# Optimization experiments

Measured on AMD Instinct MI355X. Metric: run time of the kernel, lower is better.

The kernel has to match this reference:

```python
import jax, jax.numpy as jnp
import numpy as np

B, H, S, Dqk, Dv = 4, 16, 2048, 64, 64
HID = 1024  # hidden_dim; v_tot_dim = H*Dv = 1024


def setup_inputs() -> dict:
    key = jax.random.key(0)
    kq, kk, kv, kw = jax.random.split(key, 4)
    return {
        "q": jax.random.normal(kq, (B, H, S, Dqk), dtype=jnp.float32),
        "k": jax.random.normal(kk, (B, H, S, Dqk), dtype=jnp.float32),
        "v": jax.random.normal(kv, (B, H, S, Dv), dtype=jnp.float32),
        "attention_mask": jnp.zeros((B, H, S, S), dtype=jnp.float32),
        "W_proj": jax.random.normal(kw, (HID, H * Dv), dtype=jnp.float32) * 0.02,
    }


def reference(q, k, v, attention_mask, W_proj):
    # scores: [B, H, S, S] -- explicitly materialized, as in the original
    scores = jnp.einsum("bhqd,bhkd->bhqk", q, k) + attention_mask
    attn = jax.nn.softmax(scores, axis=-1)
    # attn @ v -> [B, H, S, Dv]
    out = jnp.einsum("bhqk,bhkd->bhqd", attn, v)
    # rearrange '... h l d -> ... l (h d)'
    out = jnp.transpose(out, (0, 2, 1, 3)).reshape(B, S, H * Dv)
    # Linear(bias=False): y = x @ W^T
    out = out @ W_proj.T
    return (out, attn)
```

## Files before the change

kernel.cpp:

```cpp
#include <hip/hip_runtime.h>
#include <hip/hip_bf16.h>

#define BB 4
#define HH 16
#define SS 2048
#define DD 64
#define HIDD 1024
#define NBH (BB * HH)
#define EQK (NBH * SS * DD)
#define LOG2E 1.44269504088896f
#define M2C 57.7078016f

typedef __attribute__((ext_vector_type(4))) float f32x4;
typedef __attribute__((ext_vector_type(8))) short bf16x8;

__device__ __forceinline__ short f2bf(float x) {
    union { float f; unsigned u; } v; v.f = x;
    return (short)((v.u + 0x7FFFu + ((v.u >> 16) & 1u)) >> 16);
}
__device__ __forceinline__ float bf2f(short b) {
    union { float f; unsigned u; } v;
    v.u = ((unsigned)(unsigned short)b) << 16;
    return v.f;
}
__device__ __forceinline__ f32x4 mfma16(bf16x8 a, bf16x8 b, f32x4 c) {
    return __builtin_amdgcn_mfma_f32_16x16x32_bf16(a, b, c, 0, 0, 0);
}
__device__ __forceinline__ float fexp2(float x) { return __builtin_amdgcn_exp2f(x); }

__global__ __launch_bounds__(256) void prep_split(const float* __restrict__ k,
                                                  short* __restrict__ hi,
                                                  short* __restrict__ lo) {
    int t = blockIdx.x * 256 + threadIdx.x;
    int lane = t & 63, h = (t >> 6) & 1, kt = (t >> 7) & 127, bh = t >> 14;
    int r16 = lane & 15, gl = lane >> 4;
    int s = kt * 16 + r16, d0 = h * 32 + gl * 8;
    const float* src = k + ((size_t)bh * SS + s) * DD + d0;
    bf16x8 hh, ll;
#pragma unroll
    for (int j = 0; j < 8; ++j) {
        float x = src[j];
        short hb = f2bf(x);
        hh[j] = hb;
        ll[j] = f2bf(x - bf2f(hb));
    }
    *(bf16x8*)(hi + (size_t)t * 8) = hh;
    *(bf16x8*)(lo + (size_t)t * 8) = ll;
}

__global__ __launch_bounds__(256) void prep_cast(const float* __restrict__ src,
                                                 short* __restrict__ dst, int n8) {
    int i = blockIdx.x * 256 + threadIdx.x;
    if (i >= n8) return;
    const float* p = src + (size_t)i * 8;
    bf16x8 h;
#pragma unroll
    for (int j = 0; j < 8; ++j) h[j] = f2bf(p[j]);
    *(bf16x8*)(dst + (size_t)i * 8) = h;
}

__global__ __launch_bounds__(256) void vt_kernel(const float* __restrict__ v,
                                                 short* __restrict__ vT) {
    int t = blockIdx.x * 256 + threadIdx.x;
    int lane = t & 63, cc = (t >> 6) & 63, dt = (t >> 12) & 3, bh = t >> 14;
    int r16 = lane & 15, gl = lane >> 4;
    const float* src = v + ((size_t)bh * SS + cc * 32 + gl * 8) * DD + dt * 16 + r16;
    bf16x8 o;
#pragma unroll
    for (int j = 0; j < 8; ++j) o[j] = f2bf(src[(size_t)j * DD]);
    *(bf16x8*)(vT + (size_t)t * 8) = o;
}

template <int PLAN>
__global__ __launch_bounds__(256) void attn_sweep(
    const float* __restrict__ q,
    const short* __restrict__ khi, const short* __restrict__ klo,
    const float* __restrict__ mask, const short* __restrict__ vT,
    short* __restrict__ Pout, float* __restrict__ attn_raw,
    float* __restrict__ lrow, short* __restrict__ pvb16) {
    __shared__ short pbuf[4][2][16][40];
    const int w = threadIdx.x >> 6;
    const int lane = threadIdx.x & 63;
    const int r16 = lane & 15, g = lane >> 4;
    const int bid = blockIdx.x;
    const int swz = (bid & 7) * 256 + (bid >> 3);
    const int bh = swz >> 5;
    const int q0 = (swz & 31) * 64 + w * 16;

    const float* qrow = q + ((size_t)bh * SS + q0 + r16) * DD + g * 8;
    bf16x8 qh0, ql0, qh1, ql1;
#pragma unroll
    for (int j = 0; j < 8; ++j) {
        float x0 = qrow[j];
        short h0 = f2bf(x0); qh0[j] = h0; ql0[j] = f2bf(x0 - bf2f(h0));
        float x1 = qrow[32 + j];
        short h1 = f2bf(x1); qh1[j] = h1; ql1[j] = f2bf(x1 - bf2f(h1));
    }

    const short* kb = khi + (size_t)bh * 131072;
    const short* lb = klo + (size_t)bh * 131072;
    const float* mb = mask + ((size_t)bh * SS + q0) * SS;
    const short* vtb = vT + (size_t)bh * 131072;
    short* Pb = Pout + ((size_t)bh * SS + q0) * SS + (size_t)r16 * SS;
    float* ab = attn_raw + ((size_t)bh * SS + q0) * SS;

    float l[4] = {0.f, 0.f, 0.f, 0.f};
    f32x4 opv[4];
#pragma unroll
    for (int dt = 0; dt < 4; ++dt) opv[dt] = f32x4{0.f, 0.f, 0.f, 0.f};

    auto loadk = [&](bf16x8 (&KH)[4], bf16x8 (&KL)[4], float (&MK)[8], int ccv) {
        const short* kc = kb + (size_t)ccv * 2048 + lane * 8;
        const short* lc = lb + (size_t)ccv * 2048 + lane * 8;
#pragma unroll
        for (int u = 0; u < 4; ++u) {
            KH[u] = *(const bf16x8*)(kc + u * 512);
            KL[u] = *(const bf16x8*)(lc + u * 512);
        }
        const float* mrow = mb + ccv * 32;
#pragma unroll
        for (int i = 0; i < 4; ++i) {
            MK[2 * i]     = mrow[(size_t)(g * 4 + i) * SS + r16];
            MK[2 * i + 1] = mrow[(size_t)(g * 4 + i) * SS + 16 + r16];
        }
    };

    auto body = [&](bf16x8 (&KH)[4], bf16x8 (&KL)[4], float (&MK)[8], int ccv, int pb) {
        f32x4 a0 = {0.f, 0.f, 0.f, 0.f}, a1 = {0.f, 0.f, 0.f, 0.f};
        a0 = mfma16(qh0, KH[0], a0); a1 = mfma16(qh0, KH[2], a1);
        a0 = mfma16(ql0, KH[0], a0); a1 = mfma16(ql0, KH[2], a1);
        a0 = mfma16(qh0, KL[0], a0); a1 = mfma16(qh0, KL[2], a1);
        a0 = mfma16(qh1, KH[1], a0); a1 = mfma16(qh1, KH[3], a1);
        a0 = mfma16(ql1, KH[1], a0); a1 = mfma16(ql1, KH[3], a1);
        a0 = mfma16(qh1, KL[1], a0); a1 = mfma16(qh1, KL[3], a1);
#pragma unroll
        for (int i = 0; i < 4; ++i) {
            float c0 = __builtin_fmaf(MK[2 * i], LOG2E, -M2C);
            float c1 = __builtin_fmaf(MK[2 * i + 1], LOG2E, -M2C);
            float p0 = fexp2(__builtin_fmaf(a0[i], LOG2E, c0));
            float p1 = fexp2(__builtin_fmaf(a1[i], LOG2E, c1));
            l[i] += p0 + p1;
            if constexpr (PLAN == 1) {
                ab[(size_t)(g * 4 + i) * SS + ccv * 32 + r16] = p0;
                ab[(size_t)(g * 4 + i) * SS + ccv * 32 + 16 + r16] = p1;
            }
            pbuf[w][pb][g * 4 + i][r16] = f2bf(p0);
            pbuf[w][pb][g * 4 + i][16 + r16] = f2bf(p1);
        }
        bf16x8 pf = *(const bf16x8*)&pbuf[w][pb][r16][g * 8];
        if constexpr (PLAN == 0) {
            *(bf16x8*)(Pb + ccv * 32 + g * 8) = pf;
        }
#pragma unroll
        for (int dt = 0; dt < 4; ++dt) {
            bf16x8 vf = *(const bf16x8*)(vtb + ((size_t)dt * 64 + ccv) * 512 + lane * 8);
            opv[dt] = mfma16(pf, vf, opv[dt]);
        }
    };

    bf16x8 KhA[4], KlA[4], KhB[4], KlB[4];
    float mkA[8], mkB[8];
    loadk(KhA, KlA, mkA, 0);
    for (int cc = 0; cc < 64; cc += 2) {
        loadk(KhB, KlB, mkB, cc + 1);
        body(KhA, KlA, mkA, cc, 0);
        if (cc + 2 < 64) loadk(KhA, KlA, mkA, cc + 2);
        body(KhB, KlB, mkB, cc + 1, 1);
    }

    float linv[4];
#pragma unroll
    for (int i = 0; i < 4; ++i) {
#pragma unroll
        for (int off = 1; off < 16; off <<= 1) l[i] += __shfl_xor(l[i], off, 64);
        linv[i] = 1.0f / l[i];
    }
    if (r16 == 0) {
#pragma unroll
        for (int i = 0; i < 4; ++i) lrow[(size_t)bh * SS + q0 + g * 4 + i] = linv[i];
    }

    short* pvo = pvb16 + ((size_t)bh * SS + q0) * DD;
#pragma unroll
    for (int dt = 0; dt < 4; ++dt)
#pragma unroll
        for (int i = 0; i < 4; ++i)
            pvo[(size_t)(g * 4 + i) * DD + dt * 16 + r16] = f2bf(opv[dt][i] * linv[i]);
}

__global__ __launch_bounds__(256) void rescale_a(const short* __restrict__ P,
                                                 const float* __restrict__ lrow,
                                                 float* __restrict__ attn) {
    size_t t = (size_t)blockIdx.x * 256 + threadIdx.x;
    size_t row = t >> 8;
    int c0 = (int)(t & 255) << 3;
    float s = lrow[row];
    bf16x8 p = *(const bf16x8*)(P + row * SS + c0);
    float4 o0, o1;
    o0.x = bf2f(p[0]) * s; o0.y = bf2f(p[1]) * s; o0.z = bf2f(p[2]) * s; o0.w = bf2f(p[3]) * s;
    o1.x = bf2f(p[4]) * s; o1.y = bf2f(p[5]) * s; o1.z = bf2f(p[6]) * s; o1.w = bf2f(p[7]) * s;
    float* d = attn + row * SS + c0;
    *(float4*)d = o0;
    *(float4*)(d + 4) = o1;
}

__global__ __launch_bounds__(256) void rescale_b(float* __restrict__ attn,
                                                 const float* __restrict__ lrow) {
    size_t t = (size_t)blockIdx.x * 256 + threadIdx.x;
    size_t row = t >> 8;
    int c0 = (int)(t & 255) << 3;
    float s = lrow[row];
    float* d = attn + row * SS + c0;
    float4 a = *(float4*)d, b = *(float4*)(d + 4);
    a.x *= s; a.y *= s; a.z *= s; a.w *= s;
    b.x *= s; b.y *= s; b.z *= s; b.w *= s;
    *(float4*)d = a;
    *(float4*)(d + 4) = b;
}

__global__ __launch_bounds__(256) void proj_kernel(const short* __restrict__ xb,
                                                   const short* __restrict__ wb,
                                                   float* __restrict__ out) {
    const int w = threadIdx.x >> 6;
    const int lane = threadIdx.x & 63;
    const int r16 = lane & 15, g = lane >> 4;
    const int ww = blockIdx.x * 4 + w;
    const int nb = ww >> 4;
    const int ob = ww & 15;
    const int n0 = nb * 16;
    const int n = n0 + r16;
    const int b = n >> 11, s = n & (SS - 1);

    f32x4 acc[4];
#pragma unroll
    for (int ot = 0; ot < 4; ++ot) acc[ot] = f32x4{0.f, 0.f, 0.f, 0.f};

    for (int kk = 0; kk < HIDD / 32; ++kk) {
        const int c = kk * 32 + g * 8;
        const int h = c >> 6, d = c & 63;
        bf16x8 af = *(const bf16x8*)(xb + ((size_t)(b * HH + h) * SS + s) * DD + d);
#pragma unroll
        for (int ot = 0; ot < 4; ++ot) {
            const int o = (ob * 64) + ot * 16 + r16;
            bf16x8 bf = *(const bf16x8*)(wb + (size_t)o * HIDD + c);
            acc[ot] = mfma16(af, bf, acc[ot]);
        }
    }
#pragma unroll
    for (int ot = 0; ot < 4; ++ot)
#pragma unroll
        for (int i = 0; i < 4; ++i)
            out[(size_t)(n0 + g * 4 + i) * HIDD + (ob * 64) + ot * 16 + r16] = acc[ot][i];
}

extern "C" void kernel_launch(void* const* d_in, const int* in_sizes, int n_in,
                              void* d_out, int out_size, void* d_ws, size_t ws_size,
                              hipStream_t stream) {
    const float* q   = (const float*)d_in[0];
    const float* k   = (const float*)d_in[1];
    const float* v   = (const float*)d_in[2];
    const float* msk = (const float*)d_in[3];
    const float* Wp  = (const float*)d_in[4];

    float* out = (float*)d_out;
    float* attn_out = out + (size_t)BB * SS * HIDD;

    char* ws = (char*)d_ws;
    size_t off = 0;
    short* vT  = (short*)(ws + off); off += (size_t)EQK * 2;
    short* khi = (short*)(ws + off); off += (size_t)EQK * 2;
    short* klo = (short*)(ws + off); off += (size_t)EQK * 2;
    short* wbf = (short*)(ws + off); off += (size_t)HIDD * HIDD * 2;
    short* pvb = (short*)(ws + off); off += (size_t)EQK * 2;
    float* lrw = (float*)(ws + off); off += (size_t)NBH * SS * 4;
    short* Pbf = (short*)(ws + off);
    size_t needA = off + (size_t)NBH * SS * SS * 2;
    const bool planA = (ws_size >= needA);

    prep_split<<<EQK / 8 / 256, 256, 0, stream>>>(k, khi, klo);
    prep_cast<<<HIDD * HIDD / 8 / 256, 256, 0, stream>>>(Wp, wbf, HIDD * HIDD / 8);
    vt_kernel<<<EQK / 8 / 256, 256, 0, stream>>>(v, vT);

    const int rsblocks = (int)(((size_t)NBH * SS * SS / 8) / 256);
    if (planA) {
        attn_sweep<0><<<NBH * (SS / 64), 256, 0, stream>>>(
            q, khi, klo, msk, vT, Pbf, (float*)ws, lrw, pvb);
        rescale_a<<<rsblocks, 256, 0, stream>>>(Pbf, lrw, attn_out);
    } else {
        attn_sweep<1><<<NBH * (SS / 64), 256, 0, stream>>>(
            q, khi, klo, msk, vT, (short*)ws, attn_out, lrw, pvb);
        rescale_b<<<rsblocks, 256, 0, stream>>>(attn_out, lrw);
    }
    proj_kernel<<<(BB * SS / 16) * (HIDD / 64) / 4, 256, 0, stream>>>(pvb, wbf, out);
}
```

Measured before the change: 1.041 ms.

## Transpose QK MFMA to row-per-lane layout, replace LDS P staging with shuffles

Swaps the MFMA operand order so each lane holds four consecutive key columns of one query row. The mask can then be loaded with float4 and fed in as the accumulator init, and the attn and P stores become contiguous vector writes. The LDS round trip that re-laid out P for the PV MFMA is replaced by cross-lane shuffles, and the QK product is split into two independent accumulator chains. Row-sum reduction simplifies, and launch bounds now request two blocks per CU, which risks register spills.

```diff
diff --git a/kernel.cpp b/kernel.cpp
--- a/kernel.cpp
+++ b/kernel.cpp
@@ -23,6 +23,9 @@
     v.u = ((unsigned)(unsigned short)b) << 16;
     return v.f;
 }
+__device__ __forceinline__ int pk2(float a, float b) {
+    return ((int)(unsigned short)f2bf(b) << 16) | (int)(unsigned short)f2bf(a);
+}
 __device__ __forceinline__ f32x4 mfma16(bf16x8 a, bf16x8 b, f32x4 c) {
     return __builtin_amdgcn_mfma_f32_16x16x32_bf16(a, b, c, 0, 0, 0);
 }
@@ -72,13 +75,12 @@
 }
 
 template <int PLAN>
-__global__ __launch_bounds__(256) void attn_sweep(
+__global__ __launch_bounds__(256, 2) void attn_sweep(
     const float* __restrict__ q,
     const short* __restrict__ khi, const short* __restrict__ klo,
     const float* __restrict__ mask, const short* __restrict__ vT,
     short* __restrict__ Pout, float* __restrict__ attn_raw,
     float* __restrict__ lrow, short* __restrict__ pvb16) {
-    __shared__ short pbuf[4][2][16][40];
     const int w = threadIdx.x >> 6;
     const int lane = threadIdx.x & 63;
     const int r16 = lane & 15, g = lane >> 4;
@@ -99,93 +101,106 @@
 
     const short* kb = khi + (size_t)bh * 131072;
     const short* lb = klo + (size_t)bh * 131072;
-    const float* mb = mask + ((size_t)bh * SS + q0) * SS;
+    const float* mrow = mask + ((size_t)bh * SS + q0 + r16) * SS;
     const short* vtb = vT + (size_t)bh * 131072;
-    short* Pb = Pout + ((size_t)bh * SS + q0) * SS + (size_t)r16 * SS;
-    float* ab = attn_raw + ((size_t)bh * SS + q0) * SS;
-
-    float l[4] = {0.f, 0.f, 0.f, 0.f};
-    f32x4 opv[4];
-#pragma unroll
-    for (int dt = 0; dt < 4; ++dt) opv[dt] = f32x4{0.f, 0.f, 0.f, 0.f};
-
-    auto loadk = [&](bf16x8 (&KH)[4], bf16x8 (&KL)[4], float (&MK)[8], int ccv) {
+    short* Pb = Pout + ((size_t)bh * SS + q0 + r16) * SS;
+    float* ab = attn_raw + ((size_t)bh * SS + q0 + r16) * SS;
+
+    float lsum = 0.f;
+    f32x4 opv0 = {0.f,0.f,0.f,0.f}, opv1 = {0.f,0.f,0.f,0.f};
+    f32x4 opv2 = {0.f,0.f,0.f,0.f}, opv3 = {0.f,0.f,0.f,0.f};
+
+    auto LK = [&](bf16x8 (&KH)[4], bf16x8 (&KL)[4], float4& mk0, float4& mk1, int ccv) {
         const short* kc = kb + (size_t)ccv * 2048 + lane * 8;
         const short* lc = lb + (size_t)ccv * 2048 + lane * 8;
-#pragma unroll
-        for (int u = 0; u < 4; ++u) {
-            KH[u] = *(const bf16x8*)(kc + u * 512);
-            KL[u] = *(const bf16x8*)(lc + u * 512);
+        KH[0] = *(const bf16x8*)(kc);        KH[1] = *(const bf16x8*)(kc + 512);
+        KH[2] = *(const bf16x8*)(kc + 1024); KH[3] = *(const bf16x8*)(kc + 1536);
+        KL[0] = *(const bf16x8*)(lc);        KL[1] = *(const bf16x8*)(lc + 512);
+        KL[2] = *(const bf16x8*)(lc + 1024); KL[3] = *(const bf16x8*)(lc + 1536);
+        const float* mp = mrow + ccv * 32 + 4 * g;
+        mk0 = *(const float4*)(mp);
+        mk1 = *(const float4*)(mp + 16);
+    };
+
+    auto BODY = [&](bf16x8 (&KH)[4], bf16x8 (&KL)[4], float4 mk0, float4 mk1, int ccv) {
+        const short* vc = vtb + (size_t)ccv * 512 + lane * 8;
+        bf16x8 vf0 = *(const bf16x8*)(vc);
+        bf16x8 vf1 = *(const bf16x8*)(vc + 32768);
+        bf16x8 vf2 = *(const bf16x8*)(vc + 65536);
+        bf16x8 vf3 = *(const bf16x8*)(vc + 98304);
+        f32x4 c00 = {mk0.x, mk0.y, mk0.z, mk0.w};
+        f32x4 c10 = {mk1.x, mk1.y, mk1.z, mk1.w};
+        f32x4 c01 = {0.f,0.f,0.f,0.f}, c11 = {0.f,0.f,0.f,0.f};
+        c00 = mfma16(KH[0], qh0, c00);  c01 = mfma16(KH[1], qh1, c01);
+        c10 = mfma16(KH[2], qh0, c10);  c11 = mfma16(KH[3], qh1, c11);
+        c00 = mfma16(KL[0], qh0, c00);  c01 = mfma16(KL[1], qh1, c01);
+        c10 = mfma16(KL[2], qh0, c10);  c11 = mfma16(KL[3], qh1, c11);
+        c00 = mfma16(KH[0], ql0, c00);  c01 = mfma16(KH[1], ql1, c01);
+        c10 = mfma16(KH[2], ql0, c10);  c11 = mfma16(KH[3], ql1, c11);
+        float p0[4], p1[4];
+#pragma unroll
+        for (int i = 0; i < 4; ++i) {
+            p0[i] = fexp2(__builtin_fmaf(c00[i] + c01[i], LOG2E, -M2C));
+            p1[i] = fexp2(__builtin_fmaf(c10[i] + c11[i], LOG2E, -M2C));
         }
-        const float* mrow = mb + ccv * 32;
-#pragma unroll
-        for (int i = 0; i < 4; ++i) {
-            MK[2 * i]     = mrow[(size_t)(g * 4 + i) * SS + r16];
-            MK[2 * i + 1] = mrow[(size_t)(g * 4 + i) * SS + 16 + r16];
+        lsum += (p0[0] + p0[1]) + (p0[2] + p0[3]) + (p1[0] + p1[1]) + (p1[2] + p1[3]);
+        if constexpr (PLAN == 1) {
+            float4 s0 = {p0[0], p0[1], p0[2], p0[3]};
+            float4 s1 = {p1[0], p1[1], p1[2], p1[3]};
+            *(float4*)(ab + ccv * 32 + 4 * g) = s0;
+            *(float4*)(ab + ccv * 32 + 16 + 4 * g) = s1;
         }
-    };
-
-    auto body = [&](bf16x8 (&KH)[4], bf16x8 (&KL)[4], float (&MK)[8], int ccv, int pb) {
-        f32x4 a0 = {0.f, 0.f, 0.f, 0.f}, a1 = {0.f, 0.f, 0.f, 0.f};
-        a0 = mfma16(qh0, KH[0], a0); a1 = mfma16(qh0, KH[2], a1);
-        a0 = mfma16(ql0, KH[0], a0); a1 = mfma16(ql0, KH[2], a1);
-        a0 = mfma16(qh0, KL[0], a0); a1 = mfma16(qh0, KL[2], a1);
-        a0 = mfma16(qh1, KH[1], a0); a1 = mfma16(qh1, KH[3], a1);
-        a0 = mfma16(ql1, KH[1], a0); a1 = mfma16(ql1, KH[3], a1);
-        a0 = mfma16(qh1, KL[1], a0); a1 = mfma16(qh1, KL[3], a1);
-#pragma unroll
-        for (int i = 0; i < 4; ++i) {
-            float c0 = __builtin_fmaf(MK[2 * i], LOG2E, -M2C);
-            float c1 = __builtin_fmaf(MK[2 * i + 1], LOG2E, -M2C);
-            float p0 = fexp2(__builtin_fmaf(a0[i], LOG2E, c0));
-            float p1 = fexp2(__builtin_fmaf(a1[i], LOG2E, c1));
-            l[i] += p0 + p1;
-            if constexpr (PLAN == 1) {
-                ab[(size_t)(g * 4 + i) * SS + ccv * 32 + r16] = p0;
-                ab[(size_t)(g * 4 + i) * SS + ccv * 32 + 16 + r16] = p1;
-            }
-            pbuf[w][pb][g * 4 + i][r16] = f2bf(p0);
-            pbuf[w][pb][g * 4 + i][16 + r16] = f2bf(p1);
-        }
-        bf16x8 pf = *(const bf16x8*)&pbuf[w][pb][r16][g * 8];
+        int e0 = pk2(p0[0], p0[1]), e1 = pk2(p0[2], p0[3]);
+        int e2 = pk2(p1[0], p1[1]), e3 = pk2(p1[2], p1[3]);
+        int f0 = __shfl_xor(e0, 16), f1 = __shfl_xor(e1, 16);
+        int f2 = __shfl_xor(e2, 16), f3 = __shfl_xor(e3, 16);
+        const bool ge = (g & 1) == 0;
+        int L0 = ge ? e0 : f0, L1 = ge ? e1 : f1, L2 = ge ? f0 : e0, L3 = ge ? f1 : e1;
+        int H0 = ge ? e2 : f2, H1 = ge ? e3 : f3, H2 = ge ? f2 : e2, H3 = ge ? f3 : e3;
+        const bool lo2 = g < 2;
+        int r0 = __shfl_xor(lo2 ? H0 : L0, 32);
+        int r1 = __shfl_xor(lo2 ? H1 : L1, 32);
+        int r2 = __shfl_xor(lo2 ? H2 : L2, 32);
+        int r3 = __shfl_xor(lo2 ? H3 : L3, 32);
+        union { int i4[4]; bf16x8 v; } ua;
+        ua.i4[0] = (g == 0) ? L0 : (g == 3) ? H0 : r0;
+        ua.i4[1] = (g == 0) ? L1 : (g == 3) ? H1 : r1;
+        ua.i4[2] = (g == 0) ? L2 : (g == 3) ? H2 : r2;
+        ua.i4[3] = (g == 0) ? L3 : (g == 3) ? H3 : r3;
+        bf16x8 pf = ua.v;
         if constexpr (PLAN == 0) {
             *(bf16x8*)(Pb + ccv * 32 + g * 8) = pf;
         }
-#pragma unroll
-        for (int dt = 0; dt < 4; ++dt) {
-            bf16x8 vf = *(const bf16x8*)(vtb + ((size_t)dt * 64 + ccv) * 512 + lane * 8);
-            opv[dt] = mfma16(pf, vf, opv[dt]);
-        }
+        opv0 = mfma16(pf, vf0, opv0);
+        opv1 = mfma16(pf, vf1, opv1);
+        opv2 = mfma16(pf, vf2, opv2);
+        opv3 = mfma16(pf, vf3, opv3);
     };
 
     bf16x8 KhA[4], KlA[4], KhB[4], KlB[4];
-    float mkA[8], mkB[8];
-    loadk(KhA, KlA, mkA, 0);
+    float4 mA0, mA1, mB0, mB1;
+    LK(KhA, KlA, mA0, mA1, 0);
     for (int cc = 0; cc < 64; cc += 2) {
-        loadk(KhB, KlB, mkB, cc + 1);
-        body(KhA, KlA, mkA, cc, 0);
-        if (cc + 2 < 64) loadk(KhA, KlA, mkA, cc + 2);
-        body(KhB, KlB, mkB, cc + 1, 1);
-    }
-
-    float linv[4];
+        LK(KhB, KlB, mB0, mB1, cc + 1);
+        BODY(KhA, KlA, mA0, mA1, cc);
+        if (cc + 2 < 64) LK(KhA, KlA, mA0, mA1, cc + 2);
+        BODY(KhB, KlB, mB0, mB1, cc + 1);
+    }
+
+    lsum += __shfl_xor(lsum, 16);
+    lsum += __shfl_xor(lsum, 32);
+    const float linv = 1.0f / lsum;
+    if (g == 0) lrow[(size_t)bh * SS + q0 + r16] = linv;
+
+    short* pvo = pvb16 + ((size_t)bh * SS + q0) * DD;
 #pragma unroll
     for (int i = 0; i < 4; ++i) {
-#pragma unroll
-        for (int off = 1; off < 16; off <<= 1) l[i] += __shfl_xor(l[i], off, 64);
-        linv[i] = 1.0f / l[i];
-    }
-    if (r16 == 0) {
-#pragma unroll
-        for (int i = 0; i < 4; ++i) lrow[(size_t)bh * SS + q0 + g * 4 + i] = linv[i];
-    }
-
-    short* pvo = pvb16 + ((size_t)bh * SS + q0) * DD;
-#pragma unroll
-    for (int dt = 0; dt < 4; ++dt)
-#pragma unroll
-        for (int i = 0; i < 4; ++i)
-            pvo[(size_t)(g * 4 + i) * DD + dt * 16 + r16] = f2bf(opv[dt][i] * linv[i]);
+        float li = __shfl(linv, 4 * g + i, 64);
+        pvo[(size_t)(4 * g + i) * DD + 0  + r16] = f2bf(opv0[i] * li);
+        pvo[(size_t)(4 * g + i) * DD + 16 + r16] = f2bf(opv1[i] * li);
+        pvo[(size_t)(4 * g + i) * DD + 32 + r16] = f2bf(opv2[i] * li);
+        pvo[(size_t)(4 * g + i) * DD + 48 + r16] = f2bf(opv3[i] * li);
+    }
 }
 
 __global__ __launch_bounds__(256) void rescale_a(const short* __restrict__ P,
```

After: 1.107 ms. 6.4% more time.
